# Kernel optimization log

Hardware: AMD Instinct MI355X
Metric: run time of the kernel (lower is better)

The kernel has to match this reference:

```python
import jax, jax.numpy as jnp
import numpy as np

B, H, C = 131072, 16, 32        # batch, n_holidays, n_changepoints
HID, HP, SKU = 512, 512 // 16, 64  # hidden_dim, hidden per holiday, sku embed dim
TEMP = 0.7
TIME_MAX = 365.0
LN_EPS = 1e-3  # keras LayerNormalization default epsilon


def mish(x):
    return x * jnp.tanh(jax.nn.softplus(x))


def setup_inputs() -> dict:
    key = jax.random.key(0)
    ks = jax.random.split(key, 12)
    inputs = jax.random.uniform(ks[0], (B, H), dtype=jnp.float32) * TIME_MAX
    sku_embedding = jax.random.normal(ks[1], (B, SKU), dtype=jnp.float32)
    # per-holiday params, stacked over holiday axis
    deltas = jnp.full((H, C), TIME_MAX / C, dtype=jnp.float32)  # changepoint_deltas init
    ln_gamma = jnp.ones((H, C), dtype=jnp.float32)
    ln_beta = jnp.zeros((H, C), dtype=jnp.float32)
    attn_w = jax.random.normal(ks[2], (H,), dtype=jnp.float32) * 0.5  # Dense(1) on [...,1]
    Wh = jax.random.normal(ks[3], (H, C, HP), dtype=jnp.float32) * (1.0 / np.sqrt(C))
    Wah = jax.random.normal(ks[4], (HID, HID), dtype=jnp.float32) * (1.0 / np.sqrt(HID))
    Waa = jax.random.normal(ks[5], (HID, HID), dtype=jnp.float32) * (1.0 / np.sqrt(HID))
    Wb = jax.random.normal(ks[6], (SKU, HID), dtype=jnp.float32) * (1.0 / np.sqrt(SKU))
    Wa = jax.random.normal(ks[7], (SKU, HID), dtype=jnp.float32) * (1.0 / np.sqrt(SKU))
    Wo = jax.random.normal(ks[8], (HID, 1), dtype=jnp.float32)
    Wo = Wo / jnp.linalg.norm(Wo, axis=0, keepdims=True)  # UnitNorm(axis=0) constraint
    return {"inputs": inputs, "sku_embedding": sku_embedding, "deltas": deltas,
            "ln_gamma": ln_gamma, "ln_beta": ln_beta, "attn_w": attn_w, "Wh": Wh,
            "Wah": Wah, "Waa": Waa, "Wb": Wb, "Wa": Wa, "Wo": Wo}


def reference(inputs, sku_embedding, deltas, ln_gamma, ln_beta, attn_w, Wh, Wah, Waa, Wb, Wa, Wo):
    # ChangepointReLU (vectorised over holidays): softplus -> cumsum -> rescale to [0, 365]
    pd = jax.nn.softplus(deltas)                     # [H, C]
    cps = jnp.cumsum(pd, axis=-1)
    cps = cps / cps[:, -1:] * TIME_MAX               # time_min = 0
    feats = jax.nn.relu(inputs[:, :, None] - cps[None, :, :])  # [B, H, C]
    # per-holiday LayerNorm over changepoint axis
    mu = jnp.mean(feats, axis=-1, keepdims=True)
    var = jnp.mean((feats - mu) ** 2, axis=-1, keepdims=True)
    normed = (feats - mu) * jax.lax.rsqrt(var + LN_EPS) * ln_gamma[None] + ln_beta[None]
    # per-holiday attention: Dense(1,no bias) on [...,1] == scalar multiply per holiday
    logits = normed * attn_w[None, :, None]
    attn = jax.nn.softmax(logits / TEMP, axis=-1)    # n_changepoints > 1
    attended = normed * attn                          # [B, H, C]
    # per-holiday hidden Dense(HP, mish, no bias), then concat over holidays
    hid = mish(jnp.einsum('bhc,hcd->bhd', attended, Wh))  # [B, H, HP]
    aggregated = hid.reshape(hid.shape[0], H * HP)        # [B, HID]
    agg_hidden = mish(aggregated @ Wah)                   # [B, HID]
    agg_attn = jax.nn.softmax((agg_hidden @ Waa) / TEMP, axis=-1)
    final = agg_hidden * agg_attn                         # dropout inactive (inference)
    beta = jax.nn.sigmoid(sku_embedding @ Wb)
    alpha = sku_embedding @ Wa
    final = final * beta + alpha
    return final @ Wo                                     # [B, 1]
```

## Files before the change

### kernel.cpp

```cpp
#include <hip/hip_runtime.h>
#include <hip/hip_fp16.h>
#include <stdint.h>

#define B_TOT 131072
#define CHUNK 65536
#define NH 16
#define NC 32
#define HIDD 512

typedef unsigned short u16;
typedef __attribute__((ext_vector_type(8))) short short8;
typedef __attribute__((ext_vector_type(4))) float f32x4;
typedef __attribute__((ext_vector_type(4))) int i32x4;

#define GLLDS(g, l) __builtin_amdgcn_global_load_lds((const __attribute__((address_space(1))) unsigned int*)(g), (__attribute__((address_space(3))) unsigned int*)(l), 16, 0, 0)

__device__ __forceinline__ u16 f2bf(float x){
  unsigned u = __float_as_uint(x);
  u += 0x7fffu + ((u >> 16) & 1u);
  return (u16)(u >> 16);
}
__device__ __forceinline__ float bf2f(u16 b){ return __uint_as_float(((unsigned)b) << 16); }
__device__ __forceinline__ u16 f2h(float x){ __half h = __float2half(x); return *(u16*)&h; }
__device__ __forceinline__ float h2f(u16 b){ __half h; *(u16*)&h = b; return __half2float(h); }
__device__ __forceinline__ float mishf(float x){
  float e = __expf(fminf(x, 30.f));
  float u = 1.f + e;
  float u2 = u * u;
  return x * (u2 - 1.f) / (u2 + 1.f);
}

__global__ void prep_small(const float* __restrict__ deltas, const float* __restrict__ Wa,
                           const float* __restrict__ Wo, float* __restrict__ cps, float* __restrict__ wWo)
{
  const int t = threadIdx.x;
  if (t < NH){
    float cum[NC];
    float run = 0.f;
#pragma unroll
    for (int c = 0; c < NC; c++){
      float d = deltas[t*NC + c];
      float sp = (d > 20.f) ? d : log1pf(__expf(d));
      run += sp; cum[c] = run;
    }
    float s = 365.0f / run;
#pragma unroll
    for (int c = 0; c < NC; c++) cps[t*NC + c] = cum[c] * s;
  } else if (t >= 64 && t < 128){
    const int k = t - 64;
    float s = 0.f;
    for (int n = 0; n < HIDD; n++) s += Wa[k*HIDD + n] * Wo[n];
    wWo[k] = s;
  }
}

__global__ void prep_convert(const float* __restrict__ Wah, const float* __restrict__ Waa,
                             const float* __restrict__ Wb, const float* __restrict__ Wh,
                             u16* __restrict__ WahT, u16* __restrict__ WaaT,
                             u16* __restrict__ WbT, u16* __restrict__ WhT)
{
  int i = blockIdx.x * 256 + threadIdx.x;
  if (i < 262144){ int n = i >> 9, k = i & 511; WahT[i] = f2bf(Wah[k*512 + n]); return; }
  i -= 262144;
  if (i < 262144){ int n = i >> 9, k = i & 511; WaaT[i] = f2bf(Waa[k*512 + n]); return; }
  i -= 262144;
  if (i < 32768){ int n = i >> 6, k = i & 63; WbT[i] = f2bf(Wb[k*512 + n]); return; }
  i -= 32768;
  if (i < 16384){ int h = i >> 10, r = i & 1023, d = r >> 5, c = r & 31;
                  WhT[i] = f2bf(Wh[h*1024 + c*32 + d]); return; }
}

__global__ __launch_bounds__(256) void stage1_kernel(
    const float* __restrict__ inputs, const float* __restrict__ sku,
    const float* __restrict__ ln_g, const float* __restrict__ ln_b,
    const float* __restrict__ attnw, const float* __restrict__ cps,
    const float* __restrict__ wWo, const u16* __restrict__ WhT,
    u16* __restrict__ agg, u16* __restrict__ skub, float* __restrict__ skd)
{
  __shared__ __align__(16) float in_l[256];
  __shared__ __align__(16) float cps_l[512];
  __shared__ __align__(16) float gam_l[512];
  __shared__ __align__(16) float bet_l[512];
  __shared__ float aw_l[16];
  __shared__ __align__(16) u16 at_l[16*16*32];
  __shared__ __align__(16) u16 ot_l[16*512];

  const int t = threadIdx.x;
  const int ln = t & 63;
  const long bb = (long)blockIdx.x * 16;

  in_l[t] = inputs[bb*16 + t];
  cps_l[t] = cps[t];       cps_l[t+256] = cps[t+256];
  gam_l[t] = ln_g[t];      gam_l[t+256] = ln_g[t+256];
  bet_l[t] = ln_b[t];      bet_l[t+256] = ln_b[t+256];
  if (t < 16) aw_l[t] = attnw[t];
  {
    const f32x4 sv = *(const f32x4*)&sku[bb*64 + t*4];
    unsigned lo = (unsigned)f2bf(sv.x) | ((unsigned)f2bf(sv.y) << 16);
    unsigned hi = (unsigned)f2bf(sv.z) | ((unsigned)f2bf(sv.w) << 16);
    unsigned long long v = (unsigned long long)lo | ((unsigned long long)hi << 32);
    *(unsigned long long*)&skub[bb*64 + t*4] = v;
    const f32x4 wv4 = *(const f32x4*)&wWo[(ln & 15)*4];
    float pd = sv.x*wv4.x + sv.y*wv4.y + sv.z*wv4.z + sv.w*wv4.w;
#pragma unroll
    for (int s = 1; s < 16; s <<= 1) pd += __shfl_xor(pd, s);
    if ((ln & 15) == 0) skd[bb + (t >> 4)] = pd;
  }
  __syncthreads();

  const int h = t >> 4, bi = t & 15;
  const float x = in_l[bi*16 + h];
  float nrm[NC], pw[NC];
  float s1 = 0.f;
#pragma unroll
  for (int c = 0; c < NC; c++){ float f = fmaxf(x - cps_l[h*NC + c], 0.f); nrm[c] = f; s1 += f; }
  const float mu = s1 * (1.f/NC);
  float s2 = 0.f;
#pragma unroll
  for (int c = 0; c < NC; c++){ float d = nrm[c] - mu; s2 += d*d; }
  const float rs = rsqrtf(s2 * (1.f/NC) + 1e-3f);
  const float aw = aw_l[h] * (1.0f/0.7f);
  float lmax = -1e30f;
#pragma unroll
  for (int c = 0; c < NC; c++){
    float nv = (nrm[c] - mu) * rs * gam_l[h*NC + c] + bet_l[h*NC + c];
    nrm[c] = nv;
    lmax = fmaxf(lmax, nv * aw);
  }
  float ps = 0.f;
#pragma unroll
  for (int c = 0; c < NC; c++){ float p = __expf(nrm[c]*aw - lmax); pw[c] = p; ps += p; }
  const float invs = 1.f / ps;
#pragma unroll
  for (int c = 0; c < NC; c += 2){
    unsigned pk = (unsigned)f2bf(nrm[c]*pw[c]*invs) | ((unsigned)f2bf(nrm[c+1]*pw[c+1]*invs) << 16);
    *(unsigned*)&at_l[h*512 + bi*32 + c] = pk;
  }
  __syncthreads();

  const int wv = t >> 6;
  const int lrow = ln & 15, lq = ln >> 4;
#pragma unroll
  for (int q = 0; q < 4; q++){
    const int hh = wv*4 + q;
    short8 af  = *(const short8*)&at_l[hh*512 + lrow*32 + lq*8];
    short8 bf0 = *(const short8*)&WhT[hh*1024 + lrow*32 + lq*8];
    short8 bf1 = *(const short8*)&WhT[hh*1024 + (16 + lrow)*32 + lq*8];
    f32x4 acc0 = {0.f,0.f,0.f,0.f}, acc1 = {0.f,0.f,0.f,0.f};
    acc0 = __builtin_amdgcn_mfma_f32_16x16x32_bf16(af, bf0, acc0, 0, 0, 0);
    acc1 = __builtin_amdgcn_mfma_f32_16x16x32_bf16(af, bf1, acc1, 0, 0, 0);
#pragma unroll
    for (int r = 0; r < 4; r++){
      const int br = lq*4 + r;
      ot_l[br*512 + hh*32 + lrow]      = f2bf(mishf(acc0[r]));
      ot_l[br*512 + hh*32 + 16 + lrow] = f2bf(mishf(acc1[r]));
    }
  }
  __syncthreads();
  {
    const int row = t >> 4, c16 = t & 15;
    const i32x4* src = (const i32x4*)&ot_l[row*512 + c16*32];
    i32x4* dst = (i32x4*)&agg[(bb + row)*512 + c16*32];
#pragma unroll
    for (int j = 0; j < 4; j++) dst[j] = src[j];
  }
}

__global__ __launch_bounds__(256, 3) void gemm_bw(
    const u16* __restrict__ A, const u16* __restrict__ Bt,
    const float* __restrict__ Wo, u16* __restrict__ bw)
{
  __shared__ __align__(16) u16 As[2][128*32];
  __shared__ __align__(16) u16 Bs[2][128*32];
  const int t = threadIdx.x, wv = t >> 6, ln = t & 63;
  const int g = blockIdx.x;
  const int m_idx = (g & 7) + ((g >> 5) << 3);
  const int n_idx = (g >> 3) & 3;
  const long m0 = (long)m_idx * 128;
  const int n0 = n_idx * 128;
  const int lrow = ln & 15, lq = ln >> 4;
  const int wm = wv >> 1, wn = wv & 1;

  auto stage = [&](int buf, int kt){
#pragma unroll
    for (int p = 0; p < 2; p++){
      const int chunk = p*256 + wv*64 + ln;
      const int mm = chunk >> 2, kc = chunk & 3;
      const int kcl = kc ^ ((mm >> 1) & 3);
      GLLDS(&A[(m0 + mm)*64 + kt + kcl*8],  &As[buf][(p*256 + wv*64)*8]);
      GLLDS(&Bt[(n0 + mm)*64 + kt + kcl*8], &Bs[buf][(p*256 + wv*64)*8]);
    }
  };

  f32x4 acc[4][4] = {};
  stage(0, 0);
  for (int ks = 0; ks < 2; ks++){
    const int cur = ks & 1;
    __syncthreads();
    if (ks + 1 < 2) stage(cur ^ 1, (ks + 1)*32);
    short8 a[4], b[4];
#pragma unroll
    for (int i = 0; i < 4; i++){
      const int ra = wm*64 + i*16 + lrow;
      const int rb = wn*64 + i*16 + lrow;
      const int lqa = lq ^ ((ra >> 1) & 3);
      const int lqb = lq ^ ((rb >> 1) & 3);
      a[i] = *(const short8*)&As[cur][ra*32 + lqa*8];
      b[i] = *(const short8*)&Bs[cur][rb*32 + lqb*8];
    }
#pragma unroll
    for (int i = 0; i < 4; i++)
#pragma unroll
      for (int j = 0; j < 4; j++)
        acc[i][j] = __builtin_amdgcn_mfma_f32_16x16x32_bf16(a[i], b[j], acc[i][j], 0, 0, 0);
  }
#pragma unroll
  for (int j = 0; j < 4; j++){
    const int n = n0 + wn*64 + j*16 + lrow;
    const float wo = Wo[n];
#pragma unroll
    for (int i = 0; i < 4; i++){
#pragma unroll
      for (int r = 0; r < 4; r++){
        const long m = m0 + wm*64 + i*16 + lq*4 + r;
        const float sig = 1.f / (1.f + __expf(-acc[i][j][r]));
        bw[m*512 + n] = f2h(sig * wo);
      }
    }
  }
}

__global__ __launch_bounds__(512, 2) void gemm_mish(
    const u16* __restrict__ A, const u16* __restrict__ Bt, u16* __restrict__ aggh)
{
  __shared__ __align__(16) u16 lds[2*128*32 + 2*512*32];
  u16* As0 = lds;
  u16* Bs0 = lds + 2*128*32;
  const int t = threadIdx.x, wv = t >> 6, ln = t & 63;
  const int lrow = ln & 15, lq = ln >> 4;
  const int rh = wv >> 2, cq = wv & 3;
  const long m0 = (long)blockIdx.x * 128;

  auto stageA = [&](int buf, int kt){
    const int mm = t >> 2, kc = t & 3;
    const int kcl = kc ^ ((mm >> 1) & 3);
    GLLDS(&A[(m0 + mm)*512 + kt + kcl*8], &As0[buf*4096 + t*8]);
  };
  auto stageB = [&](int buf, int kt){
#pragma unroll
    for (int p = 0; p < 4; p++){
      const int idx = p*512 + t;
      const int mm = idx >> 2, kc = idx & 3;
      const int kcl = kc ^ ((mm >> 1) & 3);
      GLLDS(&Bt[(long)mm*512 + kt + kcl*8], &Bs0[buf*16384 + idx*8]);
    }
  };

  f32x4 acc[4][8] = {};
  stageA(0, 0); stageB(0, 0);
  for (int ks = 0; ks < 16; ks++){
    const int cur = ks & 1;
    __syncthreads();
    if (ks + 1 < 16){ stageA(cur ^ 1, (ks + 1)*32); stageB(cur ^ 1, (ks + 1)*32); }
    short8 a[4], b[8];
#pragma unroll
    for (int i = 0; i < 4; i++){
      const int ra = rh*64 + i*16 + lrow;
      const int lqa = lq ^ ((ra >> 1) & 3);
      a[i] = *(const short8*)&As0[cur*4096 + ra*32 + lqa*8];
    }
#pragma unroll
    for (int j = 0; j < 8; j++){
      const int rb = cq*128 + j*16 + lrow;
      const int lqb = lq ^ ((rb >> 1) & 3);
      b[j] = *(const short8*)&Bs0[cur*16384 + rb*32 + lqb*8];
    }
#pragma unroll
    for (int i = 0; i < 4; i++)
#pragma unroll
      for (int j = 0; j < 8; j++)
        acc[i][j] = __builtin_amdgcn_mfma_f32_16x16x32_bf16(a[i], b[j], acc[i][j], 0, 0, 0);
  }

  const int TP = 528;
  __syncthreads();
#pragma unroll 1
  for (int h = 0; h < 2; h++){
    if (rh == h){
#pragma unroll
      for (int i = 0; i < 4; i++)
#pragma unroll
        for (int j = 0; j < 8; j++)
#pragma unroll
          for (int r = 0; r < 4; r++)
            lds[(i*16 + lq*4 + r)*TP + cq*128 + j*16 + lrow] = f2bf(mishf(acc[i][j][r]));
    }
    __syncthreads();
#pragma unroll
    for (int it = 0; it < 8; it++){
      const int idx = it*512 + t;
      const int row = idx >> 6, off = idx & 63;
      const i32x4 v = *(const i32x4*)&lds[row*TP + off*8];
      *(i32x4*)&aggh[(m0 + h*64 + row)*512 + off*8] = v;
    }
    __syncthreads();
  }
}

__global__ __launch_bounds__(512, 2) void mega2(
    const u16* __restrict__ A, const u16* __restrict__ Bt,
    const u16* __restrict__ bw, const float* __restrict__ skd,
    float* __restrict__ outp)
{
  __shared__ __align__(16) u16 As[2][128*32];
  __shared__ __align__(16) u16 Bs[2][512*32];
  const int t = threadIdx.x, wv = t >> 6, ln = t & 63;
  const int lrow = ln & 15, lq = ln >> 4;
  const int rh = wv >> 2, cq = wv & 3;
  const long m0 = (long)blockIdx.x * 128;

  auto stageA = [&](int buf, int kt){
    const int mm = t >> 2, kc = t & 3;
    const int kcl = kc ^ ((mm >> 1) & 3);
    GLLDS(&A[(m0 + mm)*512 + kt + kcl*8], &As[buf][t*8]);
  };
  auto stageB = [&](int buf, int kt){
#pragma unroll
    for (int p = 0; p < 4; p++){
      const int idx = p*512 + t;
      const int mm = idx >> 2, kc = idx & 3;
      const int kcl = kc ^ ((mm >> 1) & 3);
      GLLDS(&Bt[(long)mm*512 + kt + kcl*8], &Bs[buf][idx*8]);
    }
  };

  f32x4 acc[4][8] = {};
  stageA(0, 0); stageB(0, 0);
  for (int ks = 0; ks < 16; ks++){
    const int cur = ks & 1;
    __syncthreads();
    if (ks + 1 < 16){ stageA(cur ^ 1, (ks + 1)*32); stageB(cur ^ 1, (ks + 1)*32); }
    short8 a[4], b[8];
#pragma unroll
    for (int i = 0; i < 4; i++){
      const int ra = rh*64 + i*16 + lrow;
      const int lqa = lq ^ ((ra >> 1) & 3);
      a[i] = *(const short8*)&As[cur][ra*32 + lqa*8];
    }
#pragma unroll
    for (int j = 0; j < 8; j++){
      const int rb = cq*128 + j*16 + lrow;
      const int lqb = lq ^ ((rb >> 1) & 3);
      b[j] = *(const short8*)&Bs[cur][rb*32 + lqb*8];
    }
#pragma unroll
    for (int i = 0; i < 4; i++)
#pragma unroll
      for (int j = 0; j < 8; j++)
        acc[i][j] = __builtin_amdgcn_mfma_f32_16x16x32_bf16(a[i], b[j], acc[i][j], 0, 0, 0);
  }

  __syncthreads();
  float* mxs = (float*)&Bs[0][0];
  float* sss = mxs + 512;
  float* tts = sss + 512;
  const float inv_t = 1.0f / 0.7f;

#pragma unroll
  for (int i = 0; i < 4; i++){
#pragma unroll
    for (int r = 0; r < 4; r++){
      float tm = acc[i][0][r];
#pragma unroll
      for (int j = 1; j < 8; j++) tm = fmaxf(tm, acc[i][j][r]);
#pragma unroll
      for (int s = 1; s < 16; s <<= 1) tm = fmaxf(tm, __shfl_xor(tm, s));
      if (lrow == 0) mxs[(rh*64 + i*16 + lq*4 + r)*4 + cq] = tm;
    }
  }
  __syncthreads();
#pragma unroll
  for (int i = 0; i < 4; i++){
#pragma unroll
    for (int r = 0; r < 4; r++){
      const int row = rh*64 + i*16 + lq*4 + r;
      const float gm = fmaxf(fmaxf(mxs[row*4+0], mxs[row*4+1]),
                             fmaxf(mxs[row*4+2], mxs[row*4+3]));
      float sp = 0.f, tp = 0.f;
#pragma unroll
      for (int j = 0; j < 8; j++){
        const long gi = (m0 + row)*512 + cq*128 + j*16 + lrow;
        const float e = __expf((acc[i][j][r] - gm) * inv_t);
        sp += e;
        tp += e * bf2f(A[gi]) * h2f(bw[gi]);
      }
#pragma unroll
      for (int s = 1; s < 16; s <<= 1){ sp += __shfl_xor(sp, s); tp += __shfl_xor(tp, s); }
      if (lrow == 0){ sss[row*4 + cq] = sp; tts[row*4 + cq] = tp; }
    }
  }
  __syncthreads();
  if (t < 128){
    const float S = sss[t*4] + sss[t*4+1] + sss[t*4+2] + sss[t*4+3];
    const float T = tts[t*4] + tts[t*4+1] + tts[t*4+2] + tts[t*4+3];
    outp[m0 + t] = T / S + skd[m0 + t];
  }
}

__global__ void ws_too_small(float* o, float v){ o[(long)blockIdx.x*256 + threadIdx.x] = v; }

extern "C" void kernel_launch(void* const* d_in, const int* in_sizes, int n_in,
                              void* d_out, int out_size, void* d_ws, size_t ws_size,
                              hipStream_t stream)
{
  const float* inputs = (const float*)d_in[0];
  const float* sku    = (const float*)d_in[1];
  const float* deltas = (const float*)d_in[2];
  const float* ln_g   = (const float*)d_in[3];
  const float* ln_b   = (const float*)d_in[4];
  const float* attnw  = (const float*)d_in[5];
  const float* Wh     = (const float*)d_in[6];
  const float* Wah    = (const float*)d_in[7];
  const float* Waa    = (const float*)d_in[8];
  const float* Wb     = (const float*)d_in[9];
  const float* Wa     = (const float*)d_in[10];
  const float* Wo     = (const float*)d_in[11];
  float* outp = (float*)d_out;

  const size_t OFF_CPS  = 0;
  const size_t OFF_WWO  = 2048;
  const size_t OFF_WAHT = 4096;
  const size_t OFF_WAAT = OFF_WAHT + 524288;
  const size_t OFF_WBT  = OFF_WAAT + 524288;
  const size_t OFF_WHT  = OFF_WBT  + 65536;
  const size_t OFF_SKUB = OFF_WHT  + 32768;
  const size_t OFF_SKD  = OFF_SKUB + (size_t)CHUNK*64*2;
  const size_t OFF_AGG  = OFF_SKD  + (size_t)CHUNK*4;
  const size_t OFF_BW   = OFF_AGG  + (size_t)CHUNK*512*2;
  const size_t OFF_AGH  = OFF_BW   + (size_t)CHUNK*512*2;
  const size_t NEED     = OFF_AGH  + (size_t)CHUNK*512*2;

  if (ws_size < NEED){
    hipLaunchKernelGGL(ws_too_small, dim3(B_TOT/256), dim3(256), 0, stream,
                       outp, -(float)(ws_size >> 20));
    return;
  }

  char* ws = (char*)d_ws;
  float* cps  = (float*)(ws + OFF_CPS);
  float* wWo  = (float*)(ws + OFF_WWO);
  u16* WahT   = (u16*)(ws + OFF_WAHT);
  u16* WaaT   = (u16*)(ws + OFF_WAAT);
  u16* WbT    = (u16*)(ws + OFF_WBT);
  u16* WhT    = (u16*)(ws + OFF_WHT);
  u16* skub   = (u16*)(ws + OFF_SKUB);
  float* skd  = (float*)(ws + OFF_SKD);
  u16* agg    = (u16*)(ws + OFF_AGG);
  u16* bw     = (u16*)(ws + OFF_BW);
  u16* aggh   = (u16*)(ws + OFF_AGH);

  hipLaunchKernelGGL(prep_small, dim3(1), dim3(128), 0, stream, deltas, Wa, Wo, cps, wWo);
  hipLaunchKernelGGL(prep_convert, dim3(2240), dim3(256), 0, stream,
                     Wah, Waa, Wb, Wh, WahT, WaaT, WbT, WhT);

  for (int ch = 0; ch < B_TOT / CHUNK; ch++){
    const float* in_c  = inputs + (size_t)ch * CHUNK * 16;
    const float* sku_c = sku    + (size_t)ch * CHUNK * 64;
    float* out_c       = outp   + (size_t)ch * CHUNK;

    hipLaunchKernelGGL(stage1_kernel, dim3(CHUNK/16), dim3(256), 0, stream,
                       in_c, sku_c, ln_g, ln_b, attnw, cps, wWo, WhT, agg, skub, skd);
    hipLaunchKernelGGL(gemm_bw, dim3(CHUNK/128*4), dim3(256), 0, stream,
                       skub, WbT, Wo, bw);
    hipLaunchKernelGGL(gemm_mish, dim3(CHUNK/128), dim3(512), 0, stream,
                       agg, WahT, aggh);
    hipLaunchKernelGGL(mega2, dim3(CHUNK/128), dim3(512), 0, stream,
                       aggh, WaaT, bw, skd, out_c);
  }
}
```

Baseline: 531.0 us.

## Fuse Wah, Wb and Waa GEMMs into one kernel and drop batch chunking

Merges gemm_bw, gemm_mish and mega2 into one fused kernel. The mish hidden activations and the sigmoid(sku@Wb)*Wo gate now stay in registers and LDS instead of being written to and re-read from global memory. The first GEMM's 128 rows are processed in two 64-row halves through a swizzled LDS tile for the Waa GEMM and the softmax reduction. The whole batch runs in one launch instead of two chunks, which needs a larger workspace. It uses about 152KB of LDS per block, likely one block per CU, and re-stages Wb and Waa for each half, trading occupancy for less HBM traffic.

```diff
diff --git a/kernel.cpp b/kernel.cpp
--- a/kernel.cpp
+++ b/kernel.cpp
@@ -3,12 +3,12 @@
 #include <stdint.h>
 
 #define B_TOT 131072
-#define CHUNK 65536
 #define NH 16
 #define NC 32
 #define HIDD 512
 
 typedef unsigned short u16;
+typedef unsigned int u32;
 typedef __attribute__((ext_vector_type(8))) short short8;
 typedef __attribute__((ext_vector_type(4))) float f32x4;
 typedef __attribute__((ext_vector_type(4))) int i32x4;
@@ -166,76 +166,21 @@
   }
 }
 
-__global__ __launch_bounds__(256, 3) void gemm_bw(
-    const u16* __restrict__ A, const u16* __restrict__ Bt,
-    const float* __restrict__ Wo, u16* __restrict__ bw)
+__global__ __launch_bounds__(512, 2) void fused2(
+    const u16* __restrict__ agg, const u16* __restrict__ WahT,
+    const u16* __restrict__ WaaT, const u16* __restrict__ WbT,
+    const u16* __restrict__ skub, const float* __restrict__ Wo,
+    const float* __restrict__ skd, float* __restrict__ outp)
 {
-  __shared__ __align__(16) u16 As[2][128*32];
-  __shared__ __align__(16) u16 Bs[2][128*32];
-  const int t = threadIdx.x, wv = t >> 6, ln = t & 63;
-  const int g = blockIdx.x;
-  const int m_idx = (g & 7) + ((g >> 5) << 3);
-  const int n_idx = (g >> 3) & 3;
-  const long m0 = (long)m_idx * 128;
-  const int n0 = n_idx * 128;
-  const int lrow = ln & 15, lq = ln >> 4;
-  const int wm = wv >> 1, wn = wv & 1;
-
-  auto stage = [&](int buf, int kt){
-#pragma unroll
-    for (int p = 0; p < 2; p++){
-      const int chunk = p*256 + wv*64 + ln;
-      const int mm = chunk >> 2, kc = chunk & 3;
-      const int kcl = kc ^ ((mm >> 1) & 3);
-      GLLDS(&A[(m0 + mm)*64 + kt + kcl*8],  &As[buf][(p*256 + wv*64)*8]);
-      GLLDS(&Bt[(n0 + mm)*64 + kt + kcl*8], &Bs[buf][(p*256 + wv*64)*8]);
-    }
-  };
-
-  f32x4 acc[4][4] = {};
-  stage(0, 0);
-  for (int ks = 0; ks < 2; ks++){
-    const int cur = ks & 1;
-    __syncthreads();
-    if (ks + 1 < 2) stage(cur ^ 1, (ks + 1)*32);
-    short8 a[4], b[4];
-#pragma unroll
-    for (int i = 0; i < 4; i++){
-      const int ra = wm*64 + i*16 + lrow;
-      const int rb = wn*64 + i*16 + lrow;
-      const int lqa = lq ^ ((ra >> 1) & 3);
-      const int lqb = lq ^ ((rb >> 1) & 3);
-      a[i] = *(const short8*)&As[cur][ra*32 + lqa*8];
-      b[i] = *(const short8*)&Bs[cur][rb*32 + lqb*8];
-    }
-#pragma unroll
-    for (int i = 0; i < 4; i++)
-#pragma unroll
-      for (int j = 0; j < 4; j++)
-        acc[i][j] = __builtin_amdgcn_mfma_f32_16x16x32_bf16(a[i], b[j], acc[i][j], 0, 0, 0);
-  }
-#pragma unroll
-  for (int j = 0; j < 4; j++){
-    const int n = n0 + wn*64 + j*16 + lrow;
-    const float wo = Wo[n];
-#pragma unroll
-    for (int i = 0; i < 4; i++){
-#pragma unroll
-      for (int r = 0; r < 4; r++){
-        const long m = m0 + wm*64 + i*16 + lq*4 + r;
-        const float sig = 1.f / (1.f + __expf(-acc[i][j][r]));
-        bw[m*512 + n] = f2h(sig * wo);
-      }
-    }
-  }
-}
-
-__global__ __launch_bounds__(512, 2) void gemm_mish(
-    const u16* __restrict__ A, const u16* __restrict__ Bt, u16* __restrict__ aggh)
-{
-  __shared__ __align__(16) u16 lds[2*128*32 + 2*512*32];
-  u16* As0 = lds;
-  u16* Bs0 = lds + 2*128*32;
+  __shared__ __align__(16) char smem[155648];
+  u16* BsL = (u16*)smem;
+  u16* AsA = (u16*)(smem + 65536);
+  u16* A2  = (u16*)(smem + 81920);
+  u16* A3  = (u16*)(smem + 147456);
+  float* mxs = (float*)(smem + 65536);
+  float* sss = mxs + 512;
+  float* tts = sss + 512;
+
   const int t = threadIdx.x, wv = t >> 6, ln = t & 63;
   const int lrow = ln & 15, lq = ln >> 4;
   const int rh = wv >> 2, cq = wv & 3;
@@ -244,166 +189,183 @@
   auto stageA = [&](int buf, int kt){
     const int mm = t >> 2, kc = t & 3;
     const int kcl = kc ^ ((mm >> 1) & 3);
-    GLLDS(&A[(m0 + mm)*512 + kt + kcl*8], &As0[buf*4096 + t*8]);
+    GLLDS(&agg[(m0 + mm)*512 + kt + kcl*8], &AsA[buf*4096 + t*8]);
   };
-  auto stageB = [&](int buf, int kt){
+  auto stageB = [&](const u16* src, int ldk, int buf, int kt){
 #pragma unroll
     for (int p = 0; p < 4; p++){
       const int idx = p*512 + t;
       const int mm = idx >> 2, kc = idx & 3;
       const int kcl = kc ^ ((mm >> 1) & 3);
-      GLLDS(&Bt[(long)mm*512 + kt + kcl*8], &Bs0[buf*16384 + idx*8]);
+      GLLDS(&src[(long)mm*ldk + kt + kcl*8], &BsL[buf*16384 + idx*8]);
     }
   };
 
-  f32x4 acc[4][8] = {};
-  stageA(0, 0); stageB(0, 0);
+  f32x4 acc1[4][8] = {};
+  stageA(0, 0); stageB(WahT, 512, 0, 0);
   for (int ks = 0; ks < 16; ks++){
     const int cur = ks & 1;
     __syncthreads();
-    if (ks + 1 < 16){ stageA(cur ^ 1, (ks + 1)*32); stageB(cur ^ 1, (ks + 1)*32); }
+    if (ks + 1 < 16){ stageA(cur ^ 1, (ks + 1)*32); stageB(WahT, 512, cur ^ 1, (ks + 1)*32); }
     short8 a[4], b[8];
 #pragma unroll
     for (int i = 0; i < 4; i++){
       const int ra = rh*64 + i*16 + lrow;
       const int lqa = lq ^ ((ra >> 1) & 3);
-      a[i] = *(const short8*)&As0[cur*4096 + ra*32 + lqa*8];
+      a[i] = *(const short8*)&AsA[cur*4096 + ra*32 + lqa*8];
     }
 #pragma unroll
     for (int j = 0; j < 8; j++){
       const int rb = cq*128 + j*16 + lrow;
       const int lqb = lq ^ ((rb >> 1) & 3);
-      b[j] = *(const short8*)&Bs0[cur*16384 + rb*32 + lqb*8];
+      b[j] = *(const short8*)&BsL[cur*16384 + rb*32 + lqb*8];
     }
 #pragma unroll
     for (int i = 0; i < 4; i++)
 #pragma unroll
       for (int j = 0; j < 8; j++)
-        acc[i][j] = __builtin_amdgcn_mfma_f32_16x16x32_bf16(a[i], b[j], acc[i][j], 0, 0, 0);
-  }
-
-  const int TP = 528;
-  __syncthreads();
+        acc1[i][j] = __builtin_amdgcn_mfma_f32_16x16x32_bf16(a[i], b[j], acc1[i][j], 0, 0, 0);
+  }
+
+  u32 ap[4][8][2];
+#pragma unroll
+  for (int i = 0; i < 4; i++)
+#pragma unroll
+    for (int j = 0; j < 8; j++){
+      ap[i][j][0] = (u32)f2bf(mishf(acc1[i][j][0])) | ((u32)f2bf(mishf(acc1[i][j][1])) << 16);
+      ap[i][j][1] = (u32)f2bf(mishf(acc1[i][j][2])) | ((u32)f2bf(mishf(acc1[i][j][3])) << 16);
+    }
+
+  const float inv_t = 1.0f / 0.7f;
+
 #pragma unroll 1
   for (int h = 0; h < 2; h++){
+    __syncthreads();
+
     if (rh == h){
 #pragma unroll
       for (int i = 0; i < 4; i++)
 #pragma unroll
         for (int j = 0; j < 8; j++)
 #pragma unroll
-          for (int r = 0; r < 4; r++)
-            lds[(i*16 + lq*4 + r)*TP + cq*128 + j*16 + lrow] = f2bf(mishf(acc[i][j][r]));
-    }
-    __syncthreads();
-#pragma unroll
-    for (int it = 0; it < 8; it++){
-      const int idx = it*512 + t;
-      const int row = idx >> 6, off = idx & 63;
-      const i32x4 v = *(const i32x4*)&lds[row*TP + off*8];
-      *(i32x4*)&aggh[(m0 + h*64 + row)*512 + off*8] = v;
-    }
-    __syncthreads();
-  }
-}
-
-__global__ __launch_bounds__(512, 2) void mega2(
-    const u16* __restrict__ A, const u16* __restrict__ Bt,
-    const u16* __restrict__ bw, const float* __restrict__ skd,
-    float* __restrict__ outp)
-{
-  __shared__ __align__(16) u16 As[2][128*32];
-  __shared__ __align__(16) u16 Bs[2][512*32];
-  const int t = threadIdx.x, wv = t >> 6, ln = t & 63;
-  const int lrow = ln & 15, lq = ln >> 4;
-  const int rh = wv >> 2, cq = wv & 3;
-  const long m0 = (long)blockIdx.x * 128;
-
-  auto stageA = [&](int buf, int kt){
-    const int mm = t >> 2, kc = t & 3;
-    const int kcl = kc ^ ((mm >> 1) & 3);
-    GLLDS(&A[(m0 + mm)*512 + kt + kcl*8], &As[buf][t*8]);
-  };
-  auto stageB = [&](int buf, int kt){
-#pragma unroll
-    for (int p = 0; p < 4; p++){
-      const int idx = p*512 + t;
-      const int mm = idx >> 2, kc = idx & 3;
-      const int kcl = kc ^ ((mm >> 1) & 3);
-      GLLDS(&Bt[(long)mm*512 + kt + kcl*8], &Bs[buf][idx*8]);
-    }
-  };
-
-  f32x4 acc[4][8] = {};
-  stageA(0, 0); stageB(0, 0);
-  for (int ks = 0; ks < 16; ks++){
-    const int cur = ks & 1;
-    __syncthreads();
-    if (ks + 1 < 16){ stageA(cur ^ 1, (ks + 1)*32); stageB(cur ^ 1, (ks + 1)*32); }
-    short8 a[4], b[8];
-#pragma unroll
-    for (int i = 0; i < 4; i++){
-      const int ra = rh*64 + i*16 + lrow;
-      const int lqa = lq ^ ((ra >> 1) & 3);
-      a[i] = *(const short8*)&As[cur][ra*32 + lqa*8];
-    }
-#pragma unroll
-    for (int j = 0; j < 8; j++){
-      const int rb = cq*128 + j*16 + lrow;
-      const int lqb = lq ^ ((rb >> 1) & 3);
-      b[j] = *(const short8*)&Bs[cur][rb*32 + lqb*8];
-    }
+          for (int rp = 0; rp < 2; rp++){
+            const int col = cq*128 + j*16 + lrow;
+            const int r0 = i*16 + lq*4 + rp*2;
+            const u32 pk = ap[i][j][rp];
+            A2[r0*512 + (((col >> 3) ^ (r0 & 7)) << 3) + (col & 7)] = (u16)pk;
+            A2[(r0+1)*512 + (((col >> 3) ^ ((r0+1) & 7)) << 3) + (col & 7)] = (u16)(pk >> 16);
+          }
+    }
+    {
+      const int row = t >> 3;
+      const int G = (t & 7) ^ (row & 7);
+      GLLDS(&skub[(m0 + h*64 + row)*64 + G*8], &A3[t*8]);
+    }
+    stageB(WbT, 64, 0, 0);
+    stageB(WbT, 64, 1, 32);
+    __syncthreads();
+
+    f32x4 acc3[4][4] = {};
+#pragma unroll
+    for (int ks3 = 0; ks3 < 2; ks3++){
+      short8 a3[4], b3[4];
+#pragma unroll
+      for (int i = 0; i < 4; i++){
+        const int row = i*16 + lrow;
+        a3[i] = *(const short8*)&A3[row*64 + ((((ks3 << 2) | lq) ^ (row & 7)) << 3)];
+      }
+#pragma unroll
+      for (int j = 0; j < 4; j++){
+        const int rb = wv*64 + j*16 + lrow;
+        const int lqb = lq ^ ((rb >> 1) & 3);
+        b3[j] = *(const short8*)&BsL[ks3*16384 + rb*32 + lqb*8];
+      }
+#pragma unroll
+      for (int i = 0; i < 4; i++)
+#pragma unroll
+        for (int j = 0; j < 4; j++)
+          acc3[i][j] = __builtin_amdgcn_mfma_f32_16x16x32_bf16(a3[i], b3[j], acc3[i][j], 0, 0, 0);
+    }
+    u32 bwp[4][4][2];
+#pragma unroll
+    for (int j = 0; j < 4; j++){
+      const float wo = Wo[wv*64 + j*16 + lrow];
+#pragma unroll
+      for (int i = 0; i < 4; i++)
+#pragma unroll
+        for (int rp = 0; rp < 2; rp++){
+          const float s0 = wo / (1.f + __expf(-acc3[i][j][2*rp]));
+          const float s1 = wo / (1.f + __expf(-acc3[i][j][2*rp+1]));
+          bwp[i][j][rp] = (u32)f2h(s0) | ((u32)f2h(s1) << 16);
+        }
+    }
+    __syncthreads();
+
+    f32x4 acc2[4][4] = {};
+    stageB(WaaT, 512, 0, 0);
+    for (int ks = 0; ks < 16; ks++){
+      const int cur = ks & 1;
+      __syncthreads();
+      if (ks + 1 < 16) stageB(WaaT, 512, cur ^ 1, (ks + 1)*32);
+      short8 a2[4], b2[4];
+#pragma unroll
+      for (int i = 0; i < 4; i++){
+        const int row = i*16 + lrow;
+        a2[i] = *(const short8*)&A2[row*512 + ((((ks << 2) | lq) ^ (row & 7)) << 3)];
+      }
+#pragma unroll
+      for (int j = 0; j < 4; j++){
+        const int rb = wv*64 + j*16 + lrow;
+        const int lqb = lq ^ ((rb >> 1) & 3);
+        b2[j] = *(const short8*)&BsL[cur*16384 + rb*32 + lqb*8];
+      }
+#pragma unroll
+      for (int i = 0; i < 4; i++)
+#pragma unroll
+        for (int j = 0; j < 4; j++)
+          acc2[i][j] = __builtin_amdgcn_mfma_f32_16x16x32_bf16(a2[i], b2[j], acc2[i][j], 0, 0, 0);
+    }
+
 #pragma unroll
     for (int i = 0; i < 4; i++)
 #pragma unroll
-      for (int j = 0; j < 8; j++)
-        acc[i][j] = __builtin_amdgcn_mfma_f32_16x16x32_bf16(a[i], b[j], acc[i][j], 0, 0, 0);
-  }
-
-  __syncthreads();
-  float* mxs = (float*)&Bs[0][0];
-  float* sss = mxs + 512;
-  float* tts = sss + 512;
-  const float inv_t = 1.0f / 0.7f;
-
-#pragma unroll
-  for (int i = 0; i < 4; i++){
-#pragma unroll
-    for (int r = 0; r < 4; r++){
-      float tm = acc[i][0][r];
-#pragma unroll
-      for (int j = 1; j < 8; j++) tm = fmaxf(tm, acc[i][j][r]);
-#pragma unroll
-      for (int s = 1; s < 16; s <<= 1) tm = fmaxf(tm, __shfl_xor(tm, s));
-      if (lrow == 0) mxs[(rh*64 + i*16 + lq*4 + r)*4 + cq] = tm;
-    }
-  }
-  __syncthreads();
-#pragma unroll
-  for (int i = 0; i < 4; i++){
-#pragma unroll
-    for (int r = 0; r < 4; r++){
-      const int row = rh*64 + i*16 + lq*4 + r;
-      const float gm = fmaxf(fmaxf(mxs[row*4+0], mxs[row*4+1]),
-                             fmaxf(mxs[row*4+2], mxs[row*4+3]));
-      float sp = 0.f, tp = 0.f;
-#pragma unroll
-      for (int j = 0; j < 8; j++){
-        const long gi = (m0 + row)*512 + cq*128 + j*16 + lrow;
-        const float e = __expf((acc[i][j][r] - gm) * inv_t);
-        sp += e;
-        tp += e * bf2f(A[gi]) * h2f(bw[gi]);
-      }
-#pragma unroll
-      for (int s = 1; s < 16; s <<= 1){ sp += __shfl_xor(sp, s); tp += __shfl_xor(tp, s); }
-      if (lrow == 0){ sss[row*4 + cq] = sp; tts[row*4 + cq] = tp; }
-    }
-  }
-  __syncthreads();
-  if (t < 128){
-    const float S = sss[t*4] + sss[t*4+1] + sss[t*4+2] + sss[t*4+3];
-    const float T = tts[t*4] + tts[t*4+1] + tts[t*4+2] + tts[t*4+3];
-    outp[m0 + t] = T / S + skd[m0 + t];
+      for (int r = 0; r < 4; r++){
+        float tm = acc2[i][0][r];
+#pragma unroll
+        for (int j = 1; j < 4; j++) tm = fmaxf(tm, acc2[i][j][r]);
+#pragma unroll
+        for (int s = 1; s < 16; s <<= 1) tm = fmaxf(tm, __shfl_xor(tm, s));
+        if (lrow == 0) mxs[(i*16 + lq*4 + r)*8 + wv] = tm;
+      }
+    __syncthreads();
+#pragma unroll
+    for (int i = 0; i < 4; i++)
+#pragma unroll
+      for (int r = 0; r < 4; r++){
+        const int row = i*16 + lq*4 + r;
+        float gm = mxs[row*8];
+#pragma unroll
+        for (int k = 1; k < 8; k++) gm = fmaxf(gm, mxs[row*8 + k]);
+        float sp = 0.f, tp = 0.f;
+#pragma unroll
+        for (int j = 0; j < 4; j++){
+          const int col = wv*64 + j*16 + lrow;
+          const float e = __expf((acc2[i][j][r] - gm) * inv_t);
+          const float av = bf2f(A2[row*512 + (((col >> 3) ^ (row & 7)) << 3) + (col & 7)]);
+          const u16 bh = (u16)(bwp[i][j][r >> 1] >> ((r & 1)*16));
+          sp += e; tp += e * av * h2f(bh);
+        }
+#pragma unroll
+        for (int s = 1; s < 16; s <<= 1){ sp += __shfl_xor(sp, s); tp += __shfl_xor(tp, s); }
+        if (lrow == 0){ sss[row*8 + wv] = sp; tts[row*8 + wv] = tp; }
+      }
+    __syncthreads();
+    if (t < 64){
+      float S = 0.f, T = 0.f;
+#pragma unroll
+      for (int k = 0; k < 8; k++){ S += sss[t*8 + k]; T += tts[t*8 + k]; }
+      outp[m0 + h*64 + t] = T / S + skd[m0 + h*64 + t];
+    }
   }
 }
 
@@ -434,11 +396,9 @@
   const size_t OFF_WBT  = OFF_WAAT + 524288;
   const size_t OFF_WHT  = OFF_WBT  + 65536;
   const size_t OFF_SKUB = OFF_WHT  + 32768;
-  const size_t OFF_SKD  = OFF_SKUB + (size_t)CHUNK*64*2;
-  const size_t OFF_AGG  = OFF_SKD  + (size_t)CHUNK*4;
-  const size_t OFF_BW   = OFF_AGG  + (size_t)CHUNK*512*2;
-  const size_t OFF_AGH  = OFF_BW   + (size_t)CHUNK*512*2;
-  const size_t NEED     = OFF_AGH  + (size_t)CHUNK*512*2;
+  const size_t OFF_SKD  = OFF_SKUB + (size_t)B_TOT*128;
+  const size_t OFF_AGG  = OFF_SKD  + (size_t)B_TOT*4;
+  const size_t NEED     = OFF_AGG  + (size_t)B_TOT*1024;
 
   if (ws_size < NEED){
     hipLaunchKernelGGL(ws_too_small, dim3(B_TOT/256), dim3(256), 0, stream,
@@ -456,25 +416,13 @@
   u16* skub   = (u16*)(ws + OFF_SKUB);
   float* skd  = (float*)(ws + OFF_SKD);
   u16* agg    = (u16*)(ws + OFF_AGG);
-  u16* bw     = (u16*)(ws + OFF_BW);
-  u16* aggh   = (u16*)(ws + OFF_AGH);
 
   hipLaunchKernelGGL(prep_small, dim3(1), dim3(128), 0, stream, deltas, Wa, Wo, cps, wWo);
   hipLaunchKernelGGL(prep_convert, dim3(2240), dim3(256), 0, stream,
                      Wah, Waa, Wb, Wh, WahT, WaaT, WbT, WhT);
 
-  for (int ch = 0; ch < B_TOT / CHUNK; ch++){
-    const float* in_c  = inputs + (size_t)ch * CHUNK * 16;
-    const float* sku_c = sku    + (size_t)ch * CHUNK * 64;
-    float* out_c       = outp   + (size_t)ch * CHUNK;
-
-    hipLaunchKernelGGL(stage1_kernel, dim3(CHUNK/16), dim3(256), 0, stream,
-                       in_c, sku_c, ln_g, ln_b, attnw, cps, wWo, WhT, agg, skub, skd);
-    hipLaunchKernelGGL(gemm_bw, dim3(CHUNK/128*4), dim3(256), 0, stream,
-                       skub, WbT, Wo, bw);
-    hipLaunchKernelGGL(gemm_mish, dim3(CHUNK/128), dim3(512), 0, stream,
-                       agg, WahT, aggh);
-    hipLaunchKernelGGL(mega2, dim3(CHUNK/128), dim3(512), 0, stream,
-                       aggh, WaaT, bw, skd, out_c);
-  }
-}
+  hipLaunchKernelGGL(stage1_kernel, dim3(B_TOT/16), dim3(256), 0, stream,
+                     inputs, sku, ln_g, ln_b, attnw, cps, wWo, WhT, agg, skub, skd);
+  hipLaunchKernelGGL(fused2, dim3(B_TOT/128), dim3(512), 0, stream,
+                     agg, WahT, WaaT, WbT, skub, Wo, skd, outp);
+}
```

New measurement: 1.027 ms. +93.4%, slower.

## Split 512-wide GEMM tiles into 128x128 tiles with split-N softmax combine

Applied to the files above, without the earlier changes.

Both large GEMMs (gemm_mish and mega2) now use 128x128 output tiles with 256 threads instead of 128x512 tiles with 512 threads. This quadruples the block count, cuts LDS and register use per block for higher occupancy, and adds grouped block ordering for L2 reuse. Because the row softmax now spans four N-tiles, each tile writes a partial max, sum and weighted sum to workspace and a new combine kernel merges them online. The cost is an extra launch, extra partial-result traffic, and four-fold re-reads of the A operand.

```diff
diff --git a/kernel.cpp b/kernel.cpp
--- a/kernel.cpp
+++ b/kernel.cpp
@@ -9,6 +9,7 @@
 #define HIDD 512
 
 typedef unsigned short u16;
+typedef unsigned int u32;
 typedef __attribute__((ext_vector_type(8))) short short8;
 typedef __attribute__((ext_vector_type(4))) float f32x4;
 typedef __attribute__((ext_vector_type(4))) int i32x4;
@@ -230,140 +231,130 @@
   }
 }
 
-__global__ __launch_bounds__(512, 2) void gemm_mish(
+__global__ __launch_bounds__(256) void gemm1(
     const u16* __restrict__ A, const u16* __restrict__ Bt, u16* __restrict__ aggh)
 {
-  __shared__ __align__(16) u16 lds[2*128*32 + 2*512*32];
-  u16* As0 = lds;
-  u16* Bs0 = lds + 2*128*32;
+  __shared__ __align__(16) u16 smem[16384];
   const int t = threadIdx.x, wv = t >> 6, ln = t & 63;
+  const int g = blockIdx.x;
+  const int m_idx = (g & 7) + ((g >> 5) << 3);
+  const int n_idx = (g >> 3) & 3;
+  const long m0 = (long)m_idx * 128;
+  const int n0 = n_idx * 128;
   const int lrow = ln & 15, lq = ln >> 4;
-  const int rh = wv >> 2, cq = wv & 3;
-  const long m0 = (long)blockIdx.x * 128;
-
-  auto stageA = [&](int buf, int kt){
-    const int mm = t >> 2, kc = t & 3;
-    const int kcl = kc ^ ((mm >> 1) & 3);
-    GLLDS(&A[(m0 + mm)*512 + kt + kcl*8], &As0[buf*4096 + t*8]);
+  const int wm = wv >> 1, wn = wv & 1;
+
+  auto stage = [&](int buf, int kt){
+#pragma unroll
+    for (int p = 0; p < 2; p++){
+      const int chunk = p*256 + wv*64 + ln;
+      const int mm = chunk >> 2, kc = chunk & 3;
+      const int kcl = kc ^ ((mm >> 1) & 3);
+      GLLDS(&A[(m0 + mm)*512 + kt + kcl*8],  &smem[buf*4096 + (p*256 + wv*64)*8]);
+      GLLDS(&Bt[(n0 + mm)*512 + kt + kcl*8], &smem[8192 + buf*4096 + (p*256 + wv*64)*8]);
+    }
   };
-  auto stageB = [&](int buf, int kt){
-#pragma unroll
-    for (int p = 0; p < 4; p++){
-      const int idx = p*512 + t;
-      const int mm = idx >> 2, kc = idx & 3;
-      const int kcl = kc ^ ((mm >> 1) & 3);
-      GLLDS(&Bt[(long)mm*512 + kt + kcl*8], &Bs0[buf*16384 + idx*8]);
-    }
-  };
-
-  f32x4 acc[4][8] = {};
-  stageA(0, 0); stageB(0, 0);
+
+  f32x4 acc[4][4] = {};
+  stage(0, 0);
   for (int ks = 0; ks < 16; ks++){
     const int cur = ks & 1;
     __syncthreads();
-    if (ks + 1 < 16){ stageA(cur ^ 1, (ks + 1)*32); stageB(cur ^ 1, (ks + 1)*32); }
-    short8 a[4], b[8];
+    if (ks + 1 < 16) stage(cur ^ 1, (ks + 1)*32);
+    short8 a[4], b[4];
 #pragma unroll
     for (int i = 0; i < 4; i++){
-      const int ra = rh*64 + i*16 + lrow;
+      const int ra = wm*64 + i*16 + lrow;
+      const int rb = wn*64 + i*16 + lrow;
       const int lqa = lq ^ ((ra >> 1) & 3);
-      a[i] = *(const short8*)&As0[cur*4096 + ra*32 + lqa*8];
-    }
-#pragma unroll
-    for (int j = 0; j < 8; j++){
-      const int rb = cq*128 + j*16 + lrow;
       const int lqb = lq ^ ((rb >> 1) & 3);
-      b[j] = *(const short8*)&Bs0[cur*16384 + rb*32 + lqb*8];
+      a[i] = *(const short8*)&smem[cur*4096 + ra*32 + lqa*8];
+      b[i] = *(const short8*)&smem[8192 + cur*4096 + rb*32 + lqb*8];
     }
 #pragma unroll
     for (int i = 0; i < 4; i++)
 #pragma unroll
-      for (int j = 0; j < 8; j++)
+      for (int j = 0; j < 4; j++)
         acc[i][j] = __builtin_amdgcn_mfma_f32_16x16x32_bf16(a[i], b[j], acc[i][j], 0, 0, 0);
   }
 
-  const int TP = 528;
+  const int TP = 136;
   __syncthreads();
 #pragma unroll 1
   for (int h = 0; h < 2; h++){
-    if (rh == h){
+    if (wm == h){
 #pragma unroll
       for (int i = 0; i < 4; i++)
 #pragma unroll
-        for (int j = 0; j < 8; j++)
+        for (int j = 0; j < 4; j++)
 #pragma unroll
           for (int r = 0; r < 4; r++)
-            lds[(i*16 + lq*4 + r)*TP + cq*128 + j*16 + lrow] = f2bf(mishf(acc[i][j][r]));
+            smem[(i*16 + lq*4 + r)*TP + wn*64 + j*16 + lrow] = f2bf(mishf(acc[i][j][r]));
     }
     __syncthreads();
 #pragma unroll
-    for (int it = 0; it < 8; it++){
-      const int idx = it*512 + t;
-      const int row = idx >> 6, off = idx & 63;
-      const i32x4 v = *(const i32x4*)&lds[row*TP + off*8];
-      *(i32x4*)&aggh[(m0 + h*64 + row)*512 + off*8] = v;
+    for (int it = 0; it < 4; it++){
+      const int idx = it*256 + t;
+      const int row = idx >> 4, ch = idx & 15;
+      const i32x4 v = *(const i32x4*)&smem[row*TP + ch*8];
+      *(i32x4*)&aggh[(m0 + h*64 + row)*512 + n0 + ch*8] = v;
     }
     __syncthreads();
   }
 }
 
-__global__ __launch_bounds__(512, 2) void mega2(
+__global__ __launch_bounds__(256) void mega2p(
     const u16* __restrict__ A, const u16* __restrict__ Bt,
-    const u16* __restrict__ bw, const float* __restrict__ skd,
-    float* __restrict__ outp)
-{
-  __shared__ __align__(16) u16 As[2][128*32];
-  __shared__ __align__(16) u16 Bs[2][512*32];
+    const u16* __restrict__ bw, float* __restrict__ part)
+{
+  __shared__ __align__(16) u16 smem[16384];
   const int t = threadIdx.x, wv = t >> 6, ln = t & 63;
+  const int g = blockIdx.x;
+  const int m_idx = (g & 7) + ((g >> 5) << 3);
+  const int n_idx = (g >> 3) & 3;
+  const long m0 = (long)m_idx * 128;
+  const int n0 = n_idx * 128;
   const int lrow = ln & 15, lq = ln >> 4;
-  const int rh = wv >> 2, cq = wv & 3;
-  const long m0 = (long)blockIdx.x * 128;
-
-  auto stageA = [&](int buf, int kt){
-    const int mm = t >> 2, kc = t & 3;
-    const int kcl = kc ^ ((mm >> 1) & 3);
-    GLLDS(&A[(m0 + mm)*512 + kt + kcl*8], &As[buf][t*8]);
+  const int wm = wv >> 1, wn = wv & 1;
+
+  auto stage = [&](int buf, int kt){
+#pragma unroll
+    for (int p = 0; p < 2; p++){
+      const int chunk = p*256 + wv*64 + ln;
+      const int mm = chunk >> 2, kc = chunk & 3;
+      const int kcl = kc ^ ((mm >> 1) & 3);
+      GLLDS(&A[(m0 + mm)*512 + kt + kcl*8],  &smem[buf*4096 + (p*256 + wv*64)*8]);
+      GLLDS(&Bt[(n0 + mm)*512 + kt + kcl*8], &smem[8192 + buf*4096 + (p*256 + wv*64)*8]);
+    }
   };
-  auto stageB = [&](int buf, int kt){
-#pragma unroll
-    for (int p = 0; p < 4; p++){
-      const int idx = p*512 + t;
-      const int mm = idx >> 2, kc = idx & 3;
-      const int kcl = kc ^ ((mm >> 1) & 3);
-      GLLDS(&Bt[(long)mm*512 + kt + kcl*8], &Bs[buf][idx*8]);
-    }
-  };
-
-  f32x4 acc[4][8] = {};
-  stageA(0, 0); stageB(0, 0);
+
+  f32x4 acc[4][4] = {};
+  stage(0, 0);
   for (int ks = 0; ks < 16; ks++){
     const int cur = ks & 1;
     __syncthreads();
-    if (ks + 1 < 16){ stageA(cur ^ 1, (ks + 1)*32); stageB(cur ^ 1, (ks + 1)*32); }
-    short8 a[4], b[8];
+    if (ks + 1 < 16) stage(cur ^ 1, (ks + 1)*32);
+    short8 a[4], b[4];
 #pragma unroll
     for (int i = 0; i < 4; i++){
-      const int ra = rh*64 + i*16 + lrow;
+      const int ra = wm*64 + i*16 + lrow;
+      const int rb = wn*64 + i*16 + lrow;
       const int lqa = lq ^ ((ra >> 1) & 3);
-      a[i] = *(const short8*)&As[cur][ra*32 + lqa*8];
-    }
-#pragma unroll
-    for (int j = 0; j < 8; j++){
-      const int rb = cq*128 + j*16 + lrow;
       const int lqb = lq ^ ((rb >> 1) & 3);
-      b[j] = *(const short8*)&Bs[cur][rb*32 + lqb*8];
+      a[i] = *(const short8*)&smem[cur*4096 + ra*32 + lqa*8];
+      b[i] = *(const short8*)&smem[8192 + cur*4096 + rb*32 + lqb*8];
     }
 #pragma unroll
     for (int i = 0; i < 4; i++)
 #pragma unroll
-      for (int j = 0; j < 8; j++)
+      for (int j = 0; j < 4; j++)
         acc[i][j] = __builtin_amdgcn_mfma_f32_16x16x32_bf16(a[i], b[j], acc[i][j], 0, 0, 0);
   }
 
   __syncthreads();
-  float* mxs = (float*)&Bs[0][0];
-  float* sss = mxs + 512;
-  float* tts = sss + 512;
+  float* mloc = (float*)smem;
+  float* sloc = mloc + 256;
+  float* tloc = sloc + 256;
   const float inv_t = 1.0f / 0.7f;
 
 #pragma unroll
@@ -372,39 +363,55 @@
     for (int r = 0; r < 4; r++){
       float tm = acc[i][0][r];
 #pragma unroll
-      for (int j = 1; j < 8; j++) tm = fmaxf(tm, acc[i][j][r]);
+      for (int j = 1; j < 4; j++) tm = fmaxf(tm, acc[i][j][r]);
 #pragma unroll
       for (int s = 1; s < 16; s <<= 1) tm = fmaxf(tm, __shfl_xor(tm, s));
-      if (lrow == 0) mxs[(rh*64 + i*16 + lq*4 + r)*4 + cq] = tm;
-    }
-  }
-  __syncthreads();
-#pragma unroll
-  for (int i = 0; i < 4; i++){
-#pragma unroll
-    for (int r = 0; r < 4; r++){
-      const int row = rh*64 + i*16 + lq*4 + r;
-      const float gm = fmaxf(fmaxf(mxs[row*4+0], mxs[row*4+1]),
-                             fmaxf(mxs[row*4+2], mxs[row*4+3]));
       float sp = 0.f, tp = 0.f;
 #pragma unroll
-      for (int j = 0; j < 8; j++){
-        const long gi = (m0 + row)*512 + cq*128 + j*16 + lrow;
-        const float e = __expf((acc[i][j][r] - gm) * inv_t);
+      for (int j = 0; j < 4; j++){
+        const long gi = (m0 + wm*64 + i*16 + lq*4 + r)*512 + n0 + wn*64 + j*16 + lrow;
+        const float e = __expf((acc[i][j][r] - tm) * inv_t);
         sp += e;
         tp += e * bf2f(A[gi]) * h2f(bw[gi]);
       }
 #pragma unroll
       for (int s = 1; s < 16; s <<= 1){ sp += __shfl_xor(sp, s); tp += __shfl_xor(tp, s); }
-      if (lrow == 0){ sss[row*4 + cq] = sp; tts[row*4 + cq] = tp; }
+      if (lrow == 0){
+        const int row = wm*64 + i*16 + lq*4 + r;
+        mloc[row*2 + wn] = tm; sloc[row*2 + wn] = sp; tloc[row*2 + wn] = tp;
+      }
     }
   }
   __syncthreads();
   if (t < 128){
-    const float S = sss[t*4] + sss[t*4+1] + sss[t*4+2] + sss[t*4+3];
-    const float T = tts[t*4] + tts[t*4+1] + tts[t*4+2] + tts[t*4+3];
-    outp[m0 + t] = T / S + skd[m0 + t];
-  }
+    const float ma = mloc[t*2], mb = mloc[t*2 + 1];
+    const float M = fmaxf(ma, mb);
+    const float wa = __expf((ma - M) * inv_t), wb = __expf((mb - M) * inv_t);
+    const float S = sloc[t*2]*wa + sloc[t*2 + 1]*wb;
+    const float T = tloc[t*2]*wa + tloc[t*2 + 1]*wb;
+    float* pm = part + (size_t)n_idx*3*CHUNK;
+    pm[m0 + t]           = M;
+    pm[CHUNK + m0 + t]   = S;
+    pm[2*CHUNK + m0 + t] = T;
+  }
+}
+
+__global__ __launch_bounds__(256) void combine_kernel(
+    const float* __restrict__ part, const float* __restrict__ skd, float* __restrict__ outp)
+{
+  const int row = blockIdx.x*256 + threadIdx.x;
+  const float inv_t = 1.0f / 0.7f;
+  float M = -1e30f;
+#pragma unroll
+  for (int nt = 0; nt < 4; nt++) M = fmaxf(M, part[(size_t)nt*3*CHUNK + row]);
+  float S = 0.f, T = 0.f;
+#pragma unroll
+  for (int nt = 0; nt < 4; nt++){
+    const float w = __expf((part[(size_t)nt*3*CHUNK + row] - M) * inv_t);
+    S += part[(size_t)nt*3*CHUNK + CHUNK + row] * w;
+    T += part[(size_t)nt*3*CHUNK + 2*CHUNK + row] * w;
+  }
+  outp[row] = T / S + skd[row];
 }
 
 __global__ void ws_too_small(float* o, float v){ o[(long)blockIdx.x*256 + threadIdx.x] = v; }
@@ -438,7 +445,8 @@
   const size_t OFF_AGG  = OFF_SKD  + (size_t)CHUNK*4;
   const size_t OFF_BW   = OFF_AGG  + (size_t)CHUNK*512*2;
   const size_t OFF_AGH  = OFF_BW   + (size_t)CHUNK*512*2;
-  const size_t NEED     = OFF_AGH  + (size_t)CHUNK*512*2;
+  const size_t OFF_PART = OFF_AGH  + (size_t)CHUNK*512*2;
+  const size_t NEED     = OFF_PART + (size_t)4*3*CHUNK*4;
 
   if (ws_size < NEED){
     hipLaunchKernelGGL(ws_too_small, dim3(B_TOT/256), dim3(256), 0, stream,
@@ -458,6 +466,7 @@
   u16* agg    = (u16*)(ws + OFF_AGG);
   u16* bw     = (u16*)(ws + OFF_BW);
   u16* aggh   = (u16*)(ws + OFF_AGH);
+  float* part = (float*)(ws + OFF_PART);
 
   hipLaunchKernelGGL(prep_small, dim3(1), dim3(128), 0, stream, deltas, Wa, Wo, cps, wWo);
   hipLaunchKernelGGL(prep_convert, dim3(2240), dim3(256), 0, stream,
@@ -472,9 +481,11 @@
                        in_c, sku_c, ln_g, ln_b, attnw, cps, wWo, WhT, agg, skub, skd);
     hipLaunchKernelGGL(gemm_bw, dim3(CHUNK/128*4), dim3(256), 0, stream,
                        skub, WbT, Wo, bw);
-    hipLaunchKernelGGL(gemm_mish, dim3(CHUNK/128), dim3(512), 0, stream,
+    hipLaunchKernelGGL(gemm1, dim3(CHUNK/128*4), dim3(256), 0, stream,
                        agg, WahT, aggh);
-    hipLaunchKernelGGL(mega2, dim3(CHUNK/128), dim3(512), 0, stream,
-                       aggh, WaaT, bw, skd, out_c);
-  }
-}
+    hipLaunchKernelGGL(mega2p, dim3(CHUNK/128*4), dim3(256), 0, stream,
+                       aggh, WaaT, bw, part);
+    hipLaunchKernelGGL(combine_kernel, dim3(CHUNK/256), dim3(256), 0, stream,
+                       part, skd, out_c);
+  }
+}
```

Measured after the change: 542.8 us. 2.2% more time.
